# Kernel optimization log

Hardware: AMD Instinct MI355X
Metric: run time of the kernel (lower is better)

Reference implementation:

```python
import jax, jax.numpy as jnp
import numpy as np
import math

B, S, E, H = 4, 2048, 1024, 16

def setup_inputs() -> dict:
    key = jax.random.key(0)
    k1, k2, k3 = jax.random.split(key, 3)
    scale_in = 1.0 / math.sqrt(E)
    x = jax.random.normal(k1, (B, S, E), dtype=jnp.float32)
    W_attn = jax.random.normal(k2, (E, 3 * E), dtype=jnp.float32) * scale_in
    b_attn = jnp.zeros((3 * E,), dtype=jnp.float32)
    W_proj = jax.random.normal(k3, (E, E), dtype=jnp.float32) * scale_in
    b_proj = jnp.zeros((E,), dtype=jnp.float32)
    return {"x": x, "W_attn": W_attn, "b_attn": b_attn, "W_proj": W_proj, "b_proj": b_proj}

def reference(x, W_attn, b_attn, W_proj, b_proj):
    batch, seq, emb = x.shape
    hd = emb // H  # head_dim
    qkv = x @ W_attn + b_attn                      # [B,S,3E]
    q, k, v = jnp.split(qkv, 3, axis=-1)
    # [B,S,E] -> [B,H,S,hd]
    q = q.reshape(batch, seq, H, hd).transpose(0, 2, 1, 3)
    k = k.reshape(batch, seq, H, hd).transpose(0, 2, 1, 3)
    v = v.reshape(batch, seq, H, hd).transpose(0, 2, 1, 3)
    scores = jnp.einsum('bhqd,bhkd->bhqk', q, k) * (1.0 / math.sqrt(hd))
    causal = jnp.tril(jnp.ones((seq, seq), dtype=bool))
    scores = jnp.where(causal[None, None, :, :], scores, jnp.finfo(scores.dtype).min)
    attn = jax.nn.softmax(scores, axis=-1)         # dropout p=0 -> identity
    out = jnp.einsum('bhqk,bhkd->bhqd', attn, v)   # [B,H,S,hd]
    out = out.transpose(0, 2, 1, 3).reshape(batch, seq, emb)
    return out @ W_proj + b_proj
```

## Files before the change

kernel.cpp:

```cpp
#include <hip/hip_runtime.h>

typedef __bf16 bf16;
typedef __bf16 bf16x8_t __attribute__((ext_vector_type(8)));
typedef __bf16 bf16x4_t __attribute__((ext_vector_type(4)));
typedef float f32x4_t __attribute__((ext_vector_type(4)));

#define S_ 2048
#define E_ 1024
#define HD 64
#define LOG2E 1.4426950408889634f
#define QSCALE (0.125f * LOG2E)

__device__ __forceinline__ void gl_lds16(const bf16* g, bf16* l) {
  __builtin_amdgcn_global_load_lds(
      (const __attribute__((address_space(1))) unsigned int*)g,
      (__attribute__((address_space(3))) unsigned int*)l, 16, 0, 0);
}

__global__ void cvt4(const float* __restrict__ in, bf16* __restrict__ out) {
  int i = (blockIdx.x * 256 + threadIdx.x) * 4;
  float4 v = *(const float4*)(in + i);
  bf16x4_t o = { (bf16)v.x, (bf16)v.y, (bf16)v.z, (bf16)v.w };
  *(bf16x4_t*)(out + i) = o;
}

__global__ void transpose_cvt(const float* __restrict__ in, bf16* __restrict__ out,
                              int R, int C) {
  __shared__ float tile[32][33];
  int c0 = blockIdx.x * 32, r0 = blockIdx.y * 32;
  int tx = threadIdx.x & 31, ty = threadIdx.x >> 5;
#pragma unroll
  for (int i = 0; i < 32; i += 8)
    tile[ty + i][tx] = in[(size_t)(r0 + ty + i) * C + c0 + tx];
  __syncthreads();
#pragma unroll
  for (int i = 0; i < 32; i += 8)
    out[(size_t)(c0 + ty + i) * R + r0 + tx] = (bf16)tile[tx][ty + i];
}

template <int MODE>
__global__ __launch_bounds__(256, 2)
void gemm128(const bf16* __restrict__ A, const bf16* __restrict__ Bt,
             const float* __restrict__ bias,
             bf16* __restrict__ Q, bf16* __restrict__ K, bf16* __restrict__ Vt,
             float* __restrict__ Out) {
  __shared__ __align__(16) bf16 As[128 * 64];
  __shared__ __align__(16) bf16 Bs[128 * 64];
  const int tid = threadIdx.x;
  const int wave = tid >> 6, lane = tid & 63;
  const int quad = lane >> 4, l16 = lane & 15;
  const int wm = wave >> 1, wn = wave & 1;
  const int bm = blockIdx.x, bn = blockIdx.y;

  f32x4_t acc[4][4];
#pragma unroll
  for (int i = 0; i < 4; i++)
#pragma unroll
    for (int j = 0; j < 4; j++) acc[i][j] = (f32x4_t){0.f, 0.f, 0.f, 0.f};

  for (int k0 = 0; k0 < 1024; k0 += 64) {
    __syncthreads();
#pragma unroll
    for (int it = 0; it < 4; it++) {
      int id = it * 256 + tid;
      int row = id >> 3, c = id & 7;
      int sc = (c ^ (row & 7)) * 8;
      gl_lds16(A + (size_t)(bm * 128 + row) * 1024 + k0 + sc, As + id * 8);
      gl_lds16(Bt + (size_t)(bn * 128 + row) * 1024 + k0 + sc, Bs + id * 8);
    }
    __syncthreads();
#pragma unroll
    for (int ks = 0; ks < 2; ks++) {
      bf16x8_t af[4], bfr[4];
#pragma unroll
      for (int i = 0; i < 4; i++) {
        int row = wm * 64 + i * 16 + l16;
        af[i] = *(const bf16x8_t*)&As[row * 64 + (((ks * 4 + quad) ^ (row & 7)) * 8)];
      }
#pragma unroll
      for (int j = 0; j < 4; j++) {
        int row = wn * 64 + j * 16 + l16;
        bfr[j] = *(const bf16x8_t*)&Bs[row * 64 + (((ks * 4 + quad) ^ (row & 7)) * 8)];
      }
#pragma unroll
      for (int i = 0; i < 4; i++)
#pragma unroll
        for (int j = 0; j < 4; j++)
          acc[i][j] = __builtin_amdgcn_mfma_f32_16x16x32_bf16(af[i], bfr[j], acc[i][j], 0, 0, 0);
    }
  }

  if (MODE == 0) {
#pragma unroll
    for (int j = 0; j < 4; j++) {
      int n_g = bn * 128 + wn * 64 + j * 16 + l16;
      float bv = bias[n_g];
      int which = n_g >> 10;
      int cc = n_g & 1023;
      int hh = cc >> 6, dd = cc & 63;
#pragma unroll
      for (int i = 0; i < 4; i++) {
        int m0 = bm * 128 + wm * 64 + i * 16 + quad * 4;
        int bb = m0 >> 11, ss0 = m0 & 2047;
        int bhn = bb * 16 + hh;
        if (which == 2) {
          bf16x4_t pk;
#pragma unroll
          for (int r = 0; r < 4; r++) pk[r] = (bf16)(acc[i][j][r] + bv);
          *(bf16x4_t*)&Vt[((size_t)bhn * 64 + dd) * 2048 + ss0] = pk;
        } else {
          bf16* dst = (which == 0) ? Q : K;
          float scl = (which == 0) ? QSCALE : 1.f;
#pragma unroll
          for (int r = 0; r < 4; r++)
            dst[((size_t)bhn * 2048 + ss0 + r) * 64 + dd] = (bf16)((acc[i][j][r] + bv) * scl);
        }
      }
    }
  } else {
#pragma unroll
    for (int j = 0; j < 4; j++) {
      int n_g = bn * 128 + wn * 64 + j * 16 + l16;
      float bv = bias[n_g];
#pragma unroll
      for (int i = 0; i < 4; i++) {
        int m0 = bm * 128 + wm * 64 + i * 16 + quad * 4;
#pragma unroll
        for (int r = 0; r < 4; r++)
          Out[(size_t)(m0 + r) * 1024 + n_g] = acc[i][j][r] + bv;
      }
    }
  }
}

__global__ __launch_bounds__(256, 2)
void attn_kernel(const bf16* __restrict__ Q, const bf16* __restrict__ K,
                 const bf16* __restrict__ Vt, bf16* __restrict__ O) {
  __shared__ __align__(16) bf16 Ks[128 * 64];
  __shared__ __align__(16) bf16 Vs[64 * 128];
  __shared__ __align__(16) bf16 Ps[4 * 32 * 128];
  const int tid = threadIdx.x;
  const int wave = tid >> 6, lane = tid & 63;
  const int quad = lane >> 4, l16 = lane & 15;
  const int pid = blockIdx.x, bh = blockIdx.y;
  const int b = bh >> 4, h = bh & 15;

  const bf16* Qg = Q + (size_t)bh * S_ * HD;
  const bf16* Kg = K + (size_t)bh * S_ * HD;
  const bf16* Vg = Vt + (size_t)bh * HD * S_;
  bf16* Pw = Ps + wave * 4096;

  for (int qi = 0; qi < 2; qi++) {
    const int qb = qi ? (15 - pid) : pid;
    bf16x8_t qf[2][2];
#pragma unroll
    for (int ni = 0; ni < 2; ni++)
#pragma unroll
      for (int ks = 0; ks < 2; ks++)
        qf[ni][ks] = *(const bf16x8_t*)(Qg +
            (size_t)(qb * 128 + wave * 32 + ni * 16 + l16) * HD + ks * 32 + quad * 8);

    f32x4_t o[4][2];
#pragma unroll
    for (int mi = 0; mi < 4; mi++)
#pragma unroll
      for (int ni = 0; ni < 2; ni++) o[mi][ni] = (f32x4_t){0.f, 0.f, 0.f, 0.f};
    float m_[2] = {-1e30f, -1e30f}, l_[2] = {0.f, 0.f};

    for (int kb = 0; kb <= qb; kb++) {
      __syncthreads();
      const bf16* Ksrc = Kg + (size_t)kb * 128 * HD;
#pragma unroll
      for (int it = 0; it < 4; it++) {
        int id = it * 256 + tid;
        {
          int row = id >> 3, c = id & 7;
          gl_lds16(Ksrc + row * 64 + ((c ^ (row & 7)) * 8), Ks + id * 8);
        }
        {
          int d = id >> 4, c = id & 15;
          gl_lds16(Vg + (size_t)d * S_ + kb * 128 + ((c ^ (d & 7)) * 8), Vs + id * 8);
        }
      }
      __syncthreads();

      f32x4_t sacc[8][2];
#pragma unroll
      for (int mi = 0; mi < 8; mi++)
#pragma unroll
        for (int ni = 0; ni < 2; ni++) sacc[mi][ni] = (f32x4_t){0.f, 0.f, 0.f, 0.f};
#pragma unroll
      for (int ks = 0; ks < 2; ks++)
#pragma unroll
        for (int mi = 0; mi < 8; mi++) {
          int kr = mi * 16 + l16;
          bf16x8_t kf = *(const bf16x8_t*)&Ks[kr * 64 + (((ks * 4 + quad) ^ (kr & 7)) * 8)];
          sacc[mi][0] = __builtin_amdgcn_mfma_f32_16x16x32_bf16(kf, qf[0][ks], sacc[mi][0], 0, 0, 0);
          sacc[mi][1] = __builtin_amdgcn_mfma_f32_16x16x32_bf16(kf, qf[1][ks], sacc[mi][1], 0, 0, 0);
        }

      if (kb == qb) {
#pragma unroll
        for (int mi = 0; mi < 8; mi++)
#pragma unroll
          for (int ni = 0; ni < 2; ni++) {
            int qrow = wave * 32 + ni * 16 + l16;
            int krow = mi * 16 + quad * 4;
#pragma unroll
            for (int r = 0; r < 4; r++)
              if (krow + r > qrow) sacc[mi][ni][r] = -1e30f;
          }
      }

#pragma unroll
      for (int ni = 0; ni < 2; ni++) {
        float mx = sacc[0][ni][0];
#pragma unroll
        for (int mi = 0; mi < 8; mi++)
#pragma unroll
          for (int r = 0; r < 4; r++) mx = fmaxf(mx, sacc[mi][ni][r]);
        mx = fmaxf(mx, __shfl_xor(mx, 16));
        mx = fmaxf(mx, __shfl_xor(mx, 32));
        float mnew = fmaxf(m_[ni], mx);
        float alpha = __builtin_amdgcn_exp2f(m_[ni] - mnew);
        m_[ni] = mnew;
        float rs = 0.f;
#pragma unroll
        for (int mi = 0; mi < 8; mi++)
#pragma unroll
          for (int r = 0; r < 4; r++) {
            float p = __builtin_amdgcn_exp2f(sacc[mi][ni][r] - mnew);
            sacc[mi][ni][r] = p;
            rs += p;
          }
        rs += __shfl_xor(rs, 16);
        rs += __shfl_xor(rs, 32);
        l_[ni] = alpha * l_[ni] + rs;
#pragma unroll
        for (int mi = 0; mi < 4; mi++)
#pragma unroll
          for (int r = 0; r < 4; r++) o[mi][ni][r] *= alpha;
      }

#pragma unroll
      for (int ni = 0; ni < 2; ni++) {
        int qr = ni * 16 + l16;
#pragma unroll
        for (int mi = 0; mi < 8; mi++) {
          bf16x4_t pk;
#pragma unroll
          for (int r = 0; r < 4; r++) pk[r] = (bf16)sacc[mi][ni][r];
          int c = mi * 2 + (quad >> 1);
          *(bf16x4_t*)&Pw[qr * 128 + ((c ^ (qr & 7)) * 8) + (quad & 1) * 4] = pk;
        }
      }

#pragma unroll
      for (int ks2 = 0; ks2 < 4; ks2++) {
        bf16x8_t vb[4], pa[2];
#pragma unroll
        for (int mi = 0; mi < 4; mi++) {
          int d = mi * 16 + l16;
          vb[mi] = *(const bf16x8_t*)&Vs[d * 128 + (((ks2 * 4 + quad) ^ (d & 7)) * 8)];
        }
#pragma unroll
        for (int ni = 0; ni < 2; ni++) {
          int qr = ni * 16 + l16;
          pa[ni] = *(const bf16x8_t*)&Pw[qr * 128 + (((ks2 * 4 + quad) ^ (qr & 7)) * 8)];
        }
#pragma unroll
        for (int mi = 0; mi < 4; mi++)
#pragma unroll
          for (int ni = 0; ni < 2; ni++)
            o[mi][ni] = __builtin_amdgcn_mfma_f32_16x16x32_bf16(vb[mi], pa[ni], o[mi][ni], 0, 0, 0);
      }
    }

#pragma unroll
    for (int ni = 0; ni < 2; ni++) {
      float inv = 1.0f / l_[ni];
      int q_g = qb * 128 + wave * 32 + ni * 16 + l16;
      size_t rowb = (size_t)(b * S_ + q_g) * E_ + h * HD;
#pragma unroll
      for (int mi = 0; mi < 4; mi++) {
        bf16x4_t ov;
#pragma unroll
        for (int r = 0; r < 4; r++) ov[r] = (bf16)(o[mi][ni][r] * inv);
        *(bf16x4_t*)&O[rowb + mi * 16 + quad * 4] = ov;
      }
    }
  }
}

extern "C" void kernel_launch(void* const* d_in, const int* in_sizes, int n_in,
                              void* d_out, int out_size, void* d_ws, size_t ws_size,
                              hipStream_t stream) {
  const float* x      = (const float*)d_in[0];
  const float* W_attn = (const float*)d_in[1];
  const float* b_attn = (const float*)d_in[2];
  const float* W_proj = (const float*)d_in[3];
  const float* b_proj = (const float*)d_in[4];
  float* out = (float*)d_out;

  bf16* xb  = (bf16*)d_ws;
  bf16* Wat = xb + 8388608ull;
  bf16* Wpt = Wat + 3145728ull;
  bf16* Qb  = Wpt + 1048576ull;
  bf16* Kb  = Qb + 8388608ull;
  bf16* Vtb = Kb + 8388608ull;
  bf16* AOb = xb;

  cvt4<<<8192, 256, 0, stream>>>(x, xb);
  transpose_cvt<<<dim3(96, 32), 256, 0, stream>>>(W_attn, Wat, 1024, 3072);
  transpose_cvt<<<dim3(32, 32), 256, 0, stream>>>(W_proj, Wpt, 1024, 1024);
  gemm128<0><<<dim3(64, 24), 256, 0, stream>>>(xb, Wat, b_attn, Qb, Kb, Vtb, nullptr);
  attn_kernel<<<dim3(8, 64), 256, 0, stream>>>(Qb, Kb, Vtb, AOb);
  gemm128<1><<<dim3(64, 8), 256, 0, stream>>>(AOb, Wpt, b_proj, nullptr, nullptr, nullptr, out);
}
```

Before: 245.3 us.

## Split attention key tile into halves with small padded P buffer and higher occupancy

```diff
diff --git a/kernel.cpp b/kernel.cpp
--- a/kernel.cpp
+++ b/kernel.cpp
@@ -3,6 +3,7 @@
 typedef __bf16 bf16;
 typedef __bf16 bf16x8_t __attribute__((ext_vector_type(8)));
 typedef __bf16 bf16x4_t __attribute__((ext_vector_type(4)));
+typedef __bf16 bf16x2_t __attribute__((ext_vector_type(2)));
 typedef float f32x4_t __attribute__((ext_vector_type(4)));
 
 #define S_ 2048
@@ -39,7 +40,7 @@
 }
 
 template <int MODE>
-__global__ __launch_bounds__(256, 2)
+__global__ __launch_bounds__(256, 3)
 void gemm128(const bf16* __restrict__ A, const bf16* __restrict__ Bt,
              const float* __restrict__ bias,
              bf16* __restrict__ Q, bf16* __restrict__ K, bf16* __restrict__ Vt,
@@ -133,12 +134,12 @@
   }
 }
 
-__global__ __launch_bounds__(256, 2)
+__global__ __launch_bounds__(256, 4)
 void attn_kernel(const bf16* __restrict__ Q, const bf16* __restrict__ K,
                  const bf16* __restrict__ Vt, bf16* __restrict__ O) {
   __shared__ __align__(16) bf16 Ks[128 * 64];
   __shared__ __align__(16) bf16 Vs[64 * 128];
-  __shared__ __align__(16) bf16 Ps[4 * 32 * 128];
+  __shared__ int Ps[4 * 272];
   const int tid = threadIdx.x;
   const int wave = tid >> 6, lane = tid & 63;
   const int quad = lane >> 4, l16 = lane & 15;
@@ -148,7 +149,7 @@
   const bf16* Qg = Q + (size_t)bh * S_ * HD;
   const bf16* Kg = K + (size_t)bh * S_ * HD;
   const bf16* Vg = Vt + (size_t)bh * HD * S_;
-  bf16* Pw = Ps + wave * 4096;
+  int* Pw = Ps + wave * 272;
 
   for (int qi = 0; qi < 2; qi++) {
     const int qb = qi ? (15 - pid) : pid;
@@ -184,95 +185,99 @@
       }
       __syncthreads();
 
-      f32x4_t sacc[8][2];
-#pragma unroll
-      for (int mi = 0; mi < 8; mi++)
-#pragma unroll
-        for (int ni = 0; ni < 2; ni++) sacc[mi][ni] = (f32x4_t){0.f, 0.f, 0.f, 0.f};
-#pragma unroll
-      for (int ks = 0; ks < 2; ks++)
-#pragma unroll
-        for (int mi = 0; mi < 8; mi++) {
-          int kr = mi * 16 + l16;
-          bf16x8_t kf = *(const bf16x8_t*)&Ks[kr * 64 + (((ks * 4 + quad) ^ (kr & 7)) * 8)];
-          sacc[mi][0] = __builtin_amdgcn_mfma_f32_16x16x32_bf16(kf, qf[0][ks], sacc[mi][0], 0, 0, 0);
-          sacc[mi][1] = __builtin_amdgcn_mfma_f32_16x16x32_bf16(kf, qf[1][ks], sacc[mi][1], 0, 0, 0);
-        }
-
-      if (kb == qb) {
-#pragma unroll
-        for (int mi = 0; mi < 8; mi++)
+      const bool diag = (kb == qb);
+#pragma unroll
+      for (int hh = 0; hh < 2; hh++) {
+        if (diag && hh == 1 && wave < 2) continue;
+
+        f32x4_t sacc[4][2];
+#pragma unroll
+        for (int mi = 0; mi < 4; mi++)
+#pragma unroll
+          for (int ni = 0; ni < 2; ni++) sacc[mi][ni] = (f32x4_t){0.f, 0.f, 0.f, 0.f};
+#pragma unroll
+        for (int ks = 0; ks < 2; ks++)
+#pragma unroll
+          for (int mi = 0; mi < 4; mi++) {
+            int kr = hh * 64 + mi * 16 + l16;
+            bf16x8_t kf = *(const bf16x8_t*)&Ks[kr * 64 + (((ks * 4 + quad) ^ (kr & 7)) * 8)];
+            sacc[mi][0] = __builtin_amdgcn_mfma_f32_16x16x32_bf16(kf, qf[0][ks], sacc[mi][0], 0, 0, 0);
+            sacc[mi][1] = __builtin_amdgcn_mfma_f32_16x16x32_bf16(kf, qf[1][ks], sacc[mi][1], 0, 0, 0);
+          }
+
+        if (diag) {
+#pragma unroll
+          for (int mi = 0; mi < 4; mi++)
+#pragma unroll
+            for (int ni = 0; ni < 2; ni++) {
+              int qrow = wave * 32 + ni * 16 + l16;
+              int krow = hh * 64 + mi * 16 + quad * 4;
+#pragma unroll
+              for (int r = 0; r < 4; r++)
+                if (krow + r > qrow) sacc[mi][ni][r] = -1e30f;
+            }
+        }
+
+#pragma unroll
+        for (int ni = 0; ni < 2; ni++) {
+          float mx = -1e30f;
+#pragma unroll
+          for (int mi = 0; mi < 4; mi++)
+#pragma unroll
+            for (int r = 0; r < 4; r++) mx = fmaxf(mx, sacc[mi][ni][r]);
+          mx = fmaxf(mx, __shfl_xor(mx, 16));
+          mx = fmaxf(mx, __shfl_xor(mx, 32));
+          float mnew = fmaxf(m_[ni], mx);
+          float alpha = __builtin_amdgcn_exp2f(m_[ni] - mnew);
+          m_[ni] = mnew;
+          float rs = 0.f;
+#pragma unroll
+          for (int mi = 0; mi < 4; mi++)
+#pragma unroll
+            for (int r = 0; r < 4; r++) {
+              float p = __builtin_amdgcn_exp2f(sacc[mi][ni][r] - mnew);
+              sacc[mi][ni][r] = p;
+              rs += p;
+            }
+          rs += __shfl_xor(rs, 16);
+          rs += __shfl_xor(rs, 32);
+          l_[ni] = alpha * l_[ni] + rs;
+#pragma unroll
+          for (int mi = 0; mi < 4; mi++)
+#pragma unroll
+            for (int r = 0; r < 4; r++) o[mi][ni][r] *= alpha;
+        }
+
+#pragma unroll
+        for (int ks2 = 0; ks2 < 2; ks2++) {
+          bf16x8_t vb[4];
+#pragma unroll
+          for (int mi = 0; mi < 4; mi++) {
+            int d = mi * 16 + l16;
+            vb[mi] = *(const bf16x8_t*)&Vs[d * 128 + (((hh * 8 + ks2 * 4 + quad) ^ (d & 7)) * 8)];
+          }
 #pragma unroll
           for (int ni = 0; ni < 2; ni++) {
-            int qrow = wave * 32 + ni * 16 + l16;
-            int krow = mi * 16 + quad * 4;
-#pragma unroll
-            for (int r = 0; r < 4; r++)
-              if (krow + r > qrow) sacc[mi][ni][r] = -1e30f;
+#pragma unroll
+            for (int m01 = 0; m01 < 2; m01++) {
+              int smi = ks2 * 2 + m01;
+              bf16x2_t w0 = { (bf16)sacc[smi][ni][0], (bf16)sacc[smi][ni][1] };
+              bf16x2_t w1 = { (bf16)sacc[smi][ni][2], (bf16)sacc[smi][ni][3] };
+              int cw = m01 * 8 + quad * 2;
+              Pw[l16 * 17 + cw]     = __builtin_bit_cast(int, w0);
+              Pw[l16 * 17 + cw + 1] = __builtin_bit_cast(int, w1);
+            }
+            int4 rw;
+            rw.x = Pw[l16 * 17 + quad * 4 + 0];
+            rw.y = Pw[l16 * 17 + quad * 4 + 1];
+            rw.z = Pw[l16 * 17 + quad * 4 + 2];
+            rw.w = Pw[l16 * 17 + quad * 4 + 3];
+            bf16x8_t pa = __builtin_bit_cast(bf16x8_t, rw);
+#pragma unroll
+            for (int mi = 0; mi < 4; mi++)
+              o[mi][ni] = __builtin_amdgcn_mfma_f32_16x16x32_bf16(vb[mi], pa, o[mi][ni], 0, 0, 0);
           }
-      }
-
-#pragma unroll
-      for (int ni = 0; ni < 2; ni++) {
-        float mx = sacc[0][ni][0];
-#pragma unroll
-        for (int mi = 0; mi < 8; mi++)
-#pragma unroll
-          for (int r = 0; r < 4; r++) mx = fmaxf(mx, sacc[mi][ni][r]);
-        mx = fmaxf(mx, __shfl_xor(mx, 16));
-        mx = fmaxf(mx, __shfl_xor(mx, 32));
-        float mnew = fmaxf(m_[ni], mx);
-        float alpha = __builtin_amdgcn_exp2f(m_[ni] - mnew);
-        m_[ni] = mnew;
-        float rs = 0.f;
-#pragma unroll
-        for (int mi = 0; mi < 8; mi++)
-#pragma unroll
-          for (int r = 0; r < 4; r++) {
-            float p = __builtin_amdgcn_exp2f(sacc[mi][ni][r] - mnew);
-            sacc[mi][ni][r] = p;
-            rs += p;
-          }
-        rs += __shfl_xor(rs, 16);
-        rs += __shfl_xor(rs, 32);
-        l_[ni] = alpha * l_[ni] + rs;
-#pragma unroll
-        for (int mi = 0; mi < 4; mi++)
-#pragma unroll
-          for (int r = 0; r < 4; r++) o[mi][ni][r] *= alpha;
-      }
-
-#pragma unroll
-      for (int ni = 0; ni < 2; ni++) {
-        int qr = ni * 16 + l16;
-#pragma unroll
-        for (int mi = 0; mi < 8; mi++) {
-          bf16x4_t pk;
-#pragma unroll
-          for (int r = 0; r < 4; r++) pk[r] = (bf16)sacc[mi][ni][r];
-          int c = mi * 2 + (quad >> 1);
-          *(bf16x4_t*)&Pw[qr * 128 + ((c ^ (qr & 7)) * 8) + (quad & 1) * 4] = pk;
-        }
-      }
-
-#pragma unroll
-      for (int ks2 = 0; ks2 < 4; ks2++) {
-        bf16x8_t vb[4], pa[2];
-#pragma unroll
-        for (int mi = 0; mi < 4; mi++) {
-          int d = mi * 16 + l16;
-          vb[mi] = *(const bf16x8_t*)&Vs[d * 128 + (((ks2 * 4 + quad) ^ (d & 7)) * 8)];
-        }
-#pragma unroll
-        for (int ni = 0; ni < 2; ni++) {
-          int qr = ni * 16 + l16;
-          pa[ni] = *(const bf16x8_t*)&Pw[qr * 128 + (((ks2 * 4 + quad) ^ (qr & 7)) * 8)];
-        }
-#pragma unroll
-        for (int mi = 0; mi < 4; mi++)
-#pragma unroll
-          for (int ni = 0; ni < 2; ni++)
-            o[mi][ni] = __builtin_amdgcn_mfma_f32_16x16x32_bf16(vb[mi], pa[ni], o[mi][ni], 0, 0, 0);
+        }
       }
     }
 
```

New measurement: 287.2 us. +17.1%, slower.
